# Performance work log

Hardware: AMD Instinct MI355X
Metric: run time of the kernel (lower is better)

## Reference

```python
import jax, jax.numpy as jnp
import numpy as np

B, TA, TV, D, H = 4, 1024, 1024, 512, 8
HD = D // H
SCALE = HD ** -0.5
LN_EPS = 1e-5


def setup_inputs() -> dict:
    key = jax.random.key(0)
    ks = jax.random.split(key, 16)
    init = lambda k, shape, s: (jax.random.normal(k, shape, jnp.float32) * s)
    inp = {
        'q': jax.random.normal(ks[0], (B, TA, D), jnp.float32),
        'k': jax.random.normal(ks[1], (B, TV, D), jnp.float32),
        'v': jax.random.normal(ks[2], (B, TV, D), jnp.float32),
        'guide_map': jax.random.uniform(ks[3], (B, TA, TV), jnp.float32),
        'Wq': init(ks[4], (D, D), D ** -0.5), 'bq': jnp.zeros((D,), jnp.float32),
        'Wk': init(ks[5], (D, D), D ** -0.5), 'bk': jnp.zeros((D,), jnp.float32),
        'Wv': init(ks[6], (D, D), D ** -0.5), 'bv': jnp.zeros((D,), jnp.float32),
        'Wo': init(ks[7], (D, D), D ** -0.5), 'bo': jnp.zeros((D,), jnp.float32),
        'ln_gamma': jnp.ones((D,), jnp.float32),
        'ln_beta': jnp.zeros((D,), jnp.float32),
        'gate': jnp.zeros((1,), jnp.float32),
        'bias_scale': jnp.array(10.0, jnp.float32),
    }
    return inp


def layer_norm(x, gamma, beta):
    mu = jnp.mean(x, axis=-1, keepdims=True)
    var = jnp.mean(jnp.square(x - mu), axis=-1, keepdims=True)
    return (x - mu) * jax.lax.rsqrt(var + LN_EPS) * gamma + beta


def reference(q, k, v, guide_map, Wq, bq, Wk, bk, Wv, bv, Wo, bo, ln_gamma, ln_beta, gate, bias_scale):
    # project and split heads: [B, H, T, hd]
    Q = (q @ Wq.T + bq).reshape(B, TA, H, HD).transpose(0, 2, 1, 3)
    K = (k @ Wk.T + bk).reshape(B, TV, H, HD).transpose(0, 2, 1, 3)
    V = (v @ Wv.T + bv).reshape(B, TV, H, HD).transpose(0, 2, 1, 3)
    scores = jnp.einsum('bhqd,bhkd->bhqk', Q, K) * SCALE
    # transport bias, broadcast over heads (guide_map is [B,Ta,Tv])
    transport_bias = jnp.log(guide_map + 1e-8) * jax.nn.softplus(bias_scale)
    scores = scores + transport_bias[:, None, :, :]
    attn = jax.nn.softmax(scores, axis=-1)  # dropout is identity in eval
    context = jnp.einsum('bhqk,bhkd->bhqd', attn, V)
    context = context.transpose(0, 2, 1, 3).reshape(B, TA, D)
    out = context @ Wo.T + bo
    return layer_norm(q + jax.nn.sigmoid(gate) * out, ln_gamma, ln_beta)
```

## Files before the change

kernel.cpp:

```cpp
#include <hip/hip_runtime.h>
#include <hip/hip_bf16.h>
#include <math.h>

typedef __bf16 bf16_t;
typedef _Float16 hf16_t;
typedef bf16_t bf16x8 __attribute__((ext_vector_type(8)));
typedef bf16_t bf16x4 __attribute__((ext_vector_type(4)));
typedef hf16_t hf16x8 __attribute__((ext_vector_type(8)));
typedef float f32x4 __attribute__((ext_vector_type(4)));
typedef short s16x4 __attribute__((ext_vector_type(4)));

#define B_  4
#define TA_ 1024
#define TV_ 1024
#define D_  512
#define H_  8
#define HD_ 64
#define SCALE_ 0.125f

__device__ inline void g2l16(const void* g, void* l) {
    __builtin_amdgcn_global_load_lds(
        (const __attribute__((address_space(1))) void*)g,
        (__attribute__((address_space(3))) void*)l, 16, 0, 0);
}

__device__ inline f32x4 mfma16_bf16(bf16x4 a, bf16x4 b, f32x4 c) {
    return __builtin_amdgcn_mfma_f32_16x16x16bf16_1k(
        __builtin_bit_cast(s16x4, a), __builtin_bit_cast(s16x4, b), c, 0, 0, 0);
}

__global__ __launch_bounds__(256) void prep_all(
    const float* __restrict__ G, hf16_t* __restrict__ bias_t,
    const float* __restrict__ q, const float* __restrict__ k, const float* __restrict__ v,
    const float* __restrict__ Wq, const float* __restrict__ Wk,
    const float* __restrict__ Wv, const float* __restrict__ Wo,
    bf16_t* __restrict__ qb, bf16_t* __restrict__ kb, bf16_t* __restrict__ vb,
    bf16_t* __restrict__ Wb)
{
    const int tid = threadIdx.x;
    if (blockIdx.x < 1024) {
        __shared__ float Gt[64][68];
        const int kt = blockIdx.x & 15, q64 = (blockIdx.x >> 4) & 15, b = blockIdx.x >> 8;
        const int row = tid >> 4, col4 = (tid & 15) * 4;
        #pragma unroll
        for (int it = 0; it < 4; ++it) {
            int r = it * 16 + row;
            f32x4 g = *(const f32x4*)(G + ((size_t)(b * TA_ + q64 * 64 + r)) * TV_ + kt * 64 + col4);
            *(f32x4*)&Gt[r][col4] = g;
        }
        __syncthreads();
        const int lane = tid & 63, wave = tid >> 6, quad = lane >> 4, l16 = lane & 15;
        hf16x8 lo, hi;
        #pragma unroll
        for (int ct = 0; ct < 4; ++ct) {
            #pragma unroll
            for (int r = 0; r < 4; ++r) {
                float gv = Gt[wave * 16 + l16][ct * 16 + quad * 4 + r];
                float lb = __logf(gv + 1e-8f);
                int idx = ct * 4 + r;
                if (idx < 8) lo[idx] = (hf16_t)lb; else hi[idx - 8] = (hf16_t)lb;
            }
        }
        size_t doff = ((((size_t)b * 16 + kt) * 16 + q64) * 256 + tid) * 16;
        *(hf16x8*)(bias_t + doff) = lo;
        *(hf16x8*)(bias_t + doff + 8) = hi;
    } else {
        const size_t i = ((size_t)(blockIdx.x - 1024) * 256 + tid) * 8;
        const float* src; bf16_t* dst; size_t off;
        const size_t M2 = (size_t)1 << 21;
        if (i < M2)          { src = q; dst = qb; off = i; }
        else if (i < 2 * M2) { src = k; dst = kb; off = i - M2; }
        else if (i < 3 * M2) { src = v; dst = vb; off = i - 2 * M2; }
        else {
            size_t j = i - 3 * M2;
            int wsel = (int)(j >> 18); off = j & 262143;
            src = (wsel == 0) ? Wq : (wsel == 1) ? Wk : (wsel == 2) ? Wv : Wo;
            dst = Wb + ((size_t)wsel << 18);
        }
        f32x4 a = *(const f32x4*)(src + off), c = *(const f32x4*)(src + off + 4);
        bf16x8 r;
        #pragma unroll
        for (int t = 0; t < 4; ++t) { r[t] = (bf16_t)a[t]; r[t + 4] = (bf16_t)c[t]; }
        *(bf16x8*)(dst + off) = r;
    }
}

__device__ inline void gemm128_core(
    const bf16_t* __restrict__ X, const bf16_t* __restrict__ W,
    int mbase, int nbase, bf16_t (*__restrict__ Asm)[128 * 32],
    bf16_t (*__restrict__ Bsm)[128 * 32], f32x4 acc[4][4])
{
    const int tid  = threadIdx.x;
    const int wave = tid >> 6, lane = tid & 63;
    const int quad = lane >> 4, l16 = lane & 15;
    const int wm = wave & 1, wn = wave >> 1;
    const int srow = lane >> 2;
    const int scol = (lane & 3) * 8;

    auto stage = [&](int kt, int buf) {
        const int k0 = kt * 32;
        #pragma unroll
        for (int i = 0; i < 2; ++i) {
            const int row = wave * 32 + i * 16;
            g2l16(X + (size_t)(mbase + row + srow) * D_ + k0 + scol,
                  &Asm[buf][row * 32] + (size_t)lane * 8);
            g2l16(W + (size_t)(nbase + row + srow) * D_ + k0 + scol,
                  &Bsm[buf][row * 32] + (size_t)lane * 8);
        }
    };

    stage(0, 0);
    __syncthreads();
    for (int kt = 0; kt < 16; ++kt) {
        const int buf = kt & 1;
        if (kt < 15) stage(kt + 1, buf ^ 1);
        bf16x8 af[4], bf_[4];
        #pragma unroll
        for (int t = 0; t < 4; ++t) {
            af[t]  = *(const bf16x8*)&Asm[buf][(wm * 64 + t * 16 + l16) * 32 + quad * 8];
            bf_[t] = *(const bf16x8*)&Bsm[buf][(wn * 64 + t * 16 + l16) * 32 + quad * 8];
        }
        #pragma unroll
        for (int mt = 0; mt < 4; ++mt) {
            #pragma unroll
            for (int nt = 0; nt < 4; ++nt)
                acc[mt][nt] = __builtin_amdgcn_mfma_f32_16x16x32_bf16(af[mt], bf_[nt], acc[mt][nt], 0, 0, 0);
        }
        __syncthreads();
    }
}

__global__ __launch_bounds__(256) void gemm_qkv(
    const bf16_t* __restrict__ qb, const bf16_t* __restrict__ kb, const bf16_t* __restrict__ vb,
    const bf16_t* __restrict__ Wb,
    const float* __restrict__ bq, const float* __restrict__ bk, const float* __restrict__ bv,
    bf16_t* __restrict__ Qp, bf16_t* __restrict__ Kp, bf16_t* __restrict__ Vt)
{
    __shared__ bf16_t Asm[2][128 * 32];
    __shared__ bf16_t Bsm[2][128 * 32];

    const int tid  = threadIdx.x;
    const int wave = tid >> 6, lane = tid & 63;
    const int quad = lane >> 4, l16 = lane & 15;
    const int wm = wave & 1, wn = wave >> 1;
    const int mbase = blockIdx.x * 128, nbase = blockIdx.y * 128;
    const int z = blockIdx.z;

    const bf16_t* X   = (z == 0) ? qb : (z == 1) ? kb : vb;
    const float* bias = (z == 0) ? bq : (z == 1) ? bk : bv;
    const bf16_t* W   = Wb + ((size_t)z << 18);

    f32x4 acc[4][4] = {};
    gemm128_core(X, W, mbase, nbase, Asm, Bsm, acc);

    bf16_t* out = (z == 0) ? Qp : (z == 1) ? Kp : Vt;
    #pragma unroll
    for (int mt = 0; mt < 4; ++mt) {
        #pragma unroll
        for (int nt = 0; nt < 4; ++nt) {
            #pragma unroll
            for (int r = 0; r < 4; ++r) {
                int m = mbase + wm * 64 + mt * 16 + quad * 4 + r;
                int n = nbase + wn * 64 + nt * 16 + l16;
                float val = acc[mt][nt][r] + bias[n];
                int b = m >> 10, t = m & 1023, h = n >> 6, hd = n & 63;
                if (z != 2)
                    out[(((size_t)(b * H_ + h) * TA_) + t) * HD_ + hd] = (bf16_t)val;
                else
                    out[((size_t)(b * H_ + h) * HD_ + hd) * TV_ + t] = (bf16_t)val;
            }
        }
    }
}

__global__ __launch_bounds__(512, 4) void attn_kernel(
    const bf16_t* __restrict__ Qp, const bf16_t* __restrict__ Kp,
    const bf16_t* __restrict__ Vt, const hf16_t* __restrict__ bias_t,
    const float* __restrict__ bias_scale, bf16_t* __restrict__ ctx)
{
    __shared__ bf16_t Ksm[2][2][64][72];
    __shared__ bf16_t Vsm[2][2][64][72];

    const int tid  = threadIdx.x;
    const int wave = tid >> 6, lane = tid & 63;
    const int half = wave >> 2, w4 = wave & 3;
    const int quad = lane >> 4, l16 = lane & 15;
    const int bh = blockIdx.x, b = bh >> 3, h = bh & 7;
    const int q64 = blockIdx.y;
    const int t0 = half * 8;
    const int qbase = q64 * 64 + w4 * 16;
    const int rsub = lane >> 3, csub = lane & 7;
    const int shsrc = (lane & 48) | ((lane >> 2) & 12);

    const float sp = log1pf(__expf(bias_scale[0]));

    bf16x8 aq[2];
    #pragma unroll
    for (int s = 0; s < 2; ++s)
        aq[s] = *(const bf16x8*)(Qp + ((size_t)bh * TA_ + qbase + l16) * HD_ + s * 32 + quad * 8);

    f32x4 o[4] = {};
    float m_ = -1e30f, l_ = 0.f;

    auto issue_kv = [&](int kt, bf16x8 kr[2], bf16x8 vr[2]) {
        const int kbase = kt * 64;
        #pragma unroll
        for (int i = 0; i < 2; ++i) {
            int row = w4 * 16 + i * 8 + rsub;
            kr[i] = *(const bf16x8*)(Kp + ((size_t)bh * TV_ + kbase + row) * HD_ + csub * 8);
            vr[i] = *(const bf16x8*)(Vt + ((size_t)bh * HD_ + row) * TV_ + kbase + csub * 8);
        }
    };
    auto write_kv = [&](int buf, bf16x8 kr[2], bf16x8 vr[2]) {
        #pragma unroll
        for (int i = 0; i < 2; ++i) {
            int row = w4 * 16 + i * 8 + rsub;
            *(bf16x8*)&Ksm[half][buf][row][csub * 8] = kr[i];
            *(bf16x8*)&Vsm[half][buf][row][csub * 8] = vr[i];
        }
    };

    const int tidb = (w4 << 6) | lane;
    const hf16_t* bias_base = bias_t + (((size_t)b * 16 * 16 + q64) * 256 + tidb) * 16;
    auto bias_ld = [&](int kt, hf16x8& lo, hf16x8& hi) {
        const hf16_t* bp = bias_base + (size_t)kt * 65536;
        lo = *(const hf16x8*)bp;
        hi = *(const hf16x8*)(bp + 8);
    };
    hf16x8 b0lo, b0hi, b1lo, b1hi;
    bias_ld(t0, b0lo, b0hi);
    bias_ld(t0 + 1, b1lo, b1hi);

    {
        bf16x8 kr[2], vr[2];
        issue_kv(t0, kr, vr);
        write_kv(0, kr, vr);
    }
    __syncthreads();

    auto tile_body = [&](int lk, int buf, hf16x8& slo, hf16x8& shi) {
        const int kt = t0 + lk;
        bf16x8 krn[2], vrn[2];
        if (lk < 7) issue_kv(kt + 1, krn, vrn);
        hf16x8 clo = slo, chi = shi;
        if (lk < 6) bias_ld(kt + 2, slo, shi);

        f32x4 st[4];
        #pragma unroll
        for (int ct = 0; ct < 4; ++ct) {
            f32x4 acc = {};
            #pragma unroll
            for (int s = 0; s < 2; ++s) {
                bf16x8 bk = *(const bf16x8*)&Ksm[half][buf][ct * 16 + l16][s * 32 + quad * 8];
                acc = __builtin_amdgcn_mfma_f32_16x16x32_bf16(bk, aq[s], acc, 0, 0, 0);
            }
            st[ct] = acc;
        }
        float sv[4][4], mx = -1e30f;
        #pragma unroll
        for (int ct = 0; ct < 4; ++ct) {
            #pragma unroll
            for (int r = 0; r < 4; ++r) {
                int idx = ct * 4 + r;
                float lb = (idx < 8) ? (float)clo[idx] : (float)chi[idx - 8];
                float val = fmaf(lb, sp, st[ct][r] * SCALE_);
                sv[ct][r] = val;
                mx = fmaxf(mx, val);
            }
        }
        mx = fmaxf(mx, __shfl_xor(mx, 16, 64));
        mx = fmaxf(mx, __shfl_xor(mx, 32, 64));
        float mn = fmaxf(m_, mx);
        float alpha = __expf(m_ - mn);
        m_ = mn;
        float ls = 0.f;
        #pragma unroll
        for (int ct = 0; ct < 4; ++ct) {
            #pragma unroll
            for (int r = 0; r < 4; ++r) {
                float p = __expf(sv[ct][r] - mn);
                sv[ct][r] = p;
                ls += p;
            }
        }
        ls += __shfl_xor(ls, 16, 64);
        ls += __shfl_xor(ls, 32, 64);
        l_ = l_ * alpha + ls;
        #pragma unroll
        for (int r = 0; r < 4; ++r) {
            float af = __shfl(alpha, shsrc | r, 64);
            #pragma unroll
            for (int dt = 0; dt < 4; ++dt) o[dt][r] *= af;
        }
        #pragma unroll
        for (int ct = 0; ct < 4; ++ct) {
            bf16x4 ap;
            #pragma unroll
            for (int r = 0; r < 4; ++r) ap[r] = (bf16_t)sv[ct][r];
            #pragma unroll
            for (int dt = 0; dt < 4; ++dt) {
                bf16x4 bv = *(const bf16x4*)&Vsm[half][buf][dt * 16 + l16][ct * 16 + quad * 4];
                o[dt] = mfma16_bf16(ap, bv, o[dt]);
            }
        }
        if (lk < 7) write_kv(buf ^ 1, krn, vrn);
        __syncthreads();
    };

    #pragma unroll 1
    for (int kk = 0; kk < 8; kk += 2) {
        tile_body(kk,     0, b0lo, b0hi);
        tile_body(kk + 1, 1, b1lo, b1hi);
    }

    float* cb = (float*)&Ksm[0][0][0][0];
    if (half == 1) {
        float* p = cb + (size_t)tidb * 18;
        #pragma unroll
        for (int dt = 0; dt < 4; ++dt) {
            #pragma unroll
            for (int r = 0; r < 4; ++r) p[dt * 4 + r] = o[dt][r];
        }
        p[16] = m_; p[17] = l_;
    }
    __syncthreads();
    if (half == 0) {
        const float* p = cb + (size_t)tidb * 18;
        float s0[4], s1[4];
        #pragma unroll
        for (int r = 0; r < 4; ++r) {
            float m0 = __shfl(m_, shsrc | r, 64);
            float l0 = __shfl(l_, shsrc | r, 64);
            const float* pr = cb + (size_t)((w4 << 6) | (shsrc | r)) * 18;
            float m1 = pr[16], l1 = pr[17];
            float mm = fmaxf(m0, m1);
            float e0 = __expf(m0 - mm), e1 = __expf(m1 - mm);
            float L = l0 * e0 + l1 * e1;
            s0[r] = e0 / L; s1[r] = e1 / L;
        }
        #pragma unroll
        for (int dt = 0; dt < 4; ++dt) {
            #pragma unroll
            for (int r = 0; r < 4; ++r) {
                float v = o[dt][r] * s0[r] + p[dt * 4 + r] * s1[r];
                int qrow = q64 * 64 + w4 * 16 + quad * 4 + r;
                ctx[((size_t)b * TA_ + qrow) * D_ + h * HD_ + dt * 16 + l16] = (bf16_t)v;
            }
        }
    }
}

__global__ __launch_bounds__(512) void gemm_out_ln(
    const bf16_t* __restrict__ ctx, const bf16_t* __restrict__ Wob,
    const float* __restrict__ bo, const float* __restrict__ q,
    const float* __restrict__ gamma, const float* __restrict__ beta,
    const float* __restrict__ gate, float* __restrict__ y)
{
    __shared__ bf16_t Asm[2][32 * 32];
    __shared__ bf16_t Bsm[2][512 * 32];
    __shared__ float ps[32][4], psq[32][4];

    const int tid  = threadIdx.x;
    const int wave = tid >> 6, lane = tid & 63;
    const int quad = lane >> 4, l16 = lane & 15;
    const int tg = wave & 1, nh = wave >> 1;
    const int mbase = blockIdx.x * 32;

    auto stage = [&](int kt, int buf) {
        const int k0 = kt * 32;
        #pragma unroll
        for (int j = 0; j < 4; ++j) {
            int row0 = wave * 64 + j * 16;
            g2l16(Wob + (size_t)(row0 + (lane >> 2)) * D_ + k0 + (lane & 3) * 8,
                  &Bsm[buf][row0 * 32] + (size_t)lane * 8);
        }
        if (wave < 2) {
            int row0 = wave * 16;
            g2l16(ctx + (size_t)(mbase + row0 + (lane >> 2)) * D_ + k0 + (lane & 3) * 8,
                  &Asm[buf][row0 * 32] + (size_t)lane * 8);
        }
    };

    f32x4 acc[8] = {};
    stage(0, 0);
    __syncthreads();
    for (int kt = 0; kt < 16; ++kt) {
        const int buf = kt & 1;
        if (kt < 15) stage(kt + 1, buf ^ 1);
        bf16x8 af = *(const bf16x8*)&Asm[buf][(tg * 16 + l16) * 32 + quad * 8];
        #pragma unroll
        for (int nt = 0; nt < 8; ++nt) {
            bf16x8 bf_ = *(const bf16x8*)&Bsm[buf][(nh * 128 + nt * 16 + l16) * 32 + quad * 8];
            acc[nt] = __builtin_amdgcn_mfma_f32_16x16x32_bf16(af, bf_, acc[nt], 0, 0, 0);
        }
        __syncthreads();
    }

    const float sg = 1.f / (1.f + __expf(-gate[0]));
    float s[4] = {0.f, 0.f, 0.f, 0.f}, sq[4] = {0.f, 0.f, 0.f, 0.f};
    #pragma unroll
    for (int nt = 0; nt < 8; ++nt) {
        int n = nh * 128 + nt * 16 + l16;
        float bon = bo[n];
        #pragma unroll
        for (int r = 0; r < 4; ++r) {
            int m = mbase + tg * 16 + quad * 4 + r;
            float x = q[(size_t)m * D_ + n] + sg * (acc[nt][r] + bon);
            acc[nt][r] = x;
            s[r] += x; sq[r] += x * x;
        }
    }
    #pragma unroll
    for (int off = 1; off < 16; off <<= 1) {
        #pragma unroll
        for (int r = 0; r < 4; ++r) {
            s[r]  += __shfl_xor(s[r],  off, 64);
            sq[r] += __shfl_xor(sq[r], off, 64);
        }
    }
    if (l16 == 0) {
        #pragma unroll
        for (int r = 0; r < 4; ++r) {
            ps[tg * 16 + quad * 4 + r][nh]  = s[r];
            psq[tg * 16 + quad * 4 + r][nh] = sq[r];
        }
    }
    __syncthreads();
    float mu[4], rstd[4];
    #pragma unroll
    for (int r = 0; r < 4; ++r) {
        int row = tg * 16 + quad * 4 + r;
        float S  = ps[row][0] + ps[row][1] + ps[row][2] + ps[row][3];
        float SQ = psq[row][0] + psq[row][1] + psq[row][2] + psq[row][3];
        mu[r] = S * (1.f / D_);
        float var = SQ * (1.f / D_) - mu[r] * mu[r];
        rstd[r] = rsqrtf(var + 1e-5f);
    }
    #pragma unroll
    for (int nt = 0; nt < 8; ++nt) {
        int n = nh * 128 + nt * 16 + l16;
        float gn = gamma[n], bn = beta[n];
        #pragma unroll
        for (int r = 0; r < 4; ++r) {
            int m = mbase + tg * 16 + quad * 4 + r;
            y[(size_t)m * D_ + n] = (acc[nt][r] - mu[r]) * rstd[r] * gn + bn;
        }
    }
}

extern "C" void kernel_launch(void* const* d_in, const int* in_sizes, int n_in,
                              void* d_out, int out_size, void* d_ws, size_t ws_size,
                              hipStream_t stream) {
    const float* q       = (const float*)d_in[0];
    const float* k       = (const float*)d_in[1];
    const float* v       = (const float*)d_in[2];
    const float* guide   = (const float*)d_in[3];
    const float* Wq      = (const float*)d_in[4];
    const float* bq      = (const float*)d_in[5];
    const float* Wk      = (const float*)d_in[6];
    const float* bk      = (const float*)d_in[7];
    const float* Wv      = (const float*)d_in[8];
    const float* bv      = (const float*)d_in[9];
    const float* Wo      = (const float*)d_in[10];
    const float* bo      = (const float*)d_in[11];
    const float* gamma   = (const float*)d_in[12];
    const float* beta    = (const float*)d_in[13];
    const float* gate    = (const float*)d_in[14];
    const float* bscale  = (const float*)d_in[15];

    char* w = (char*)d_ws;
    bf16_t* qb     = (bf16_t*)(w);
    bf16_t* kb     = (bf16_t*)(w + (4u  << 20));
    bf16_t* vb     = (bf16_t*)(w + (8u  << 20));
    bf16_t* Wb     = (bf16_t*)(w + (12u << 20));
    bf16_t* Qp     = (bf16_t*)(w + (14u << 20));
    bf16_t* Kp     = (bf16_t*)(w + (18u << 20));
    bf16_t* Vt     = (bf16_t*)(w + (22u << 20));
    bf16_t* ctx    = (bf16_t*)(w + (26u << 20));
    hf16_t* bias_t = (hf16_t*)(w + (30u << 20));

    prep_all<<<4608, 256, 0, stream>>>(guide, bias_t, q, k, v, Wq, Wk, Wv, Wo, qb, kb, vb, Wb);
    gemm_qkv<<<dim3(32, 4, 3), 256, 0, stream>>>(qb, kb, vb, Wb, bq, bk, bv, Qp, Kp, Vt);
    attn_kernel<<<dim3(32, 16), 512, 0, stream>>>(Qp, Kp, Vt, bias_t, bscale, ctx);
    gemm_out_ln<<<128, 512, 0, stream>>>(ctx, Wb + ((size_t)3 << 18), bo, q,
                                         gamma, beta, gate, (float*)d_out);
}
```

Baseline: 176.0 us.

## Fold softmax scale into Q, use exp2, defer rescaling, prioritize MFMA waves

Q projection output is pre-multiplied by scale*log2e, and the bias multiplier also absorbs log2e, so the softmax can use a raw exp2 instruction without a per-element scale. Online-softmax rescaling of the accumulator is skipped unless the running max grows past a threshold in some lane of the wave. MFMA sections get raised wave priority, and the V-transposed store in the projection epilogue is vectorized to bf16x4. Deferring the max update risks bf16 overflow or precision loss if scores exceed the threshold range, and storing Q pre-scaled changes its bf16 rounding.

```diff
diff --git a/kernel.cpp b/kernel.cpp
--- a/kernel.cpp
+++ b/kernel.cpp
@@ -17,6 +17,11 @@
 #define H_  8
 #define HD_ 64
 #define SCALE_ 0.125f
+#define LOG2E_ 1.442695041f
+#define QSCALE_ 0.1803368801f
+#define DEFER_THR_ 11.5416f
+
+__device__ inline float fast_exp2(float x) { return __builtin_amdgcn_exp2f(x); }
 
 __device__ inline void g2l16(const void* g, void* l) {
     __builtin_amdgcn_global_load_lds(
@@ -158,16 +163,24 @@
     for (int mt = 0; mt < 4; ++mt) {
         #pragma unroll
         for (int nt = 0; nt < 4; ++nt) {
-            #pragma unroll
-            for (int r = 0; r < 4; ++r) {
-                int m = mbase + wm * 64 + mt * 16 + quad * 4 + r;
-                int n = nbase + wn * 64 + nt * 16 + l16;
-                float val = acc[mt][nt][r] + bias[n];
-                int b = m >> 10, t = m & 1023, h = n >> 6, hd = n & 63;
-                if (z != 2)
+            const int n = nbase + wn * 64 + nt * 16 + l16;
+            const float bn = bias[n];
+            if (z == 2) {
+                int m0 = mbase + wm * 64 + mt * 16 + quad * 4;
+                int b = m0 >> 10, t = m0 & 1023, h = n >> 6, hd = n & 63;
+                bf16x4 pk;
+                #pragma unroll
+                for (int r = 0; r < 4; ++r) pk[r] = (bf16_t)(acc[mt][nt][r] + bn);
+                *(bf16x4*)(out + ((size_t)(b * H_ + h) * HD_ + hd) * TV_ + t) = pk;
+            } else {
+                #pragma unroll
+                for (int r = 0; r < 4; ++r) {
+                    int m = mbase + wm * 64 + mt * 16 + quad * 4 + r;
+                    float val = acc[mt][nt][r] + bn;
+                    if (z == 0) val *= QSCALE_;
+                    int b = m >> 10, t = m & 1023, h = n >> 6, hd = n & 63;
                     out[(((size_t)(b * H_ + h) * TA_) + t) * HD_ + hd] = (bf16_t)val;
-                else
-                    out[((size_t)(b * H_ + h) * HD_ + hd) * TV_ + t] = (bf16_t)val;
+                }
             }
         }
     }
@@ -192,7 +205,7 @@
     const int rsub = lane >> 3, csub = lane & 7;
     const int shsrc = (lane & 48) | ((lane >> 2) & 12);
 
-    const float sp = log1pf(__expf(bias_scale[0]));
+    const float sp = log1pf(__expf(bias_scale[0])) * LOG2E_;
 
     bf16x8 aq[2];
     #pragma unroll
@@ -246,6 +259,7 @@
         if (lk < 6) bias_ld(kt + 2, slo, shi);
 
         f32x4 st[4];
+        __builtin_amdgcn_s_setprio(1);
         #pragma unroll
         for (int ct = 0; ct < 4; ++ct) {
             f32x4 acc = {};
@@ -256,6 +270,7 @@
             }
             st[ct] = acc;
         }
+        __builtin_amdgcn_s_setprio(0);
         float sv[4][4], mx = -1e30f;
         #pragma unroll
         for (int ct = 0; ct < 4; ++ct) {
@@ -263,35 +278,42 @@
             for (int r = 0; r < 4; ++r) {
                 int idx = ct * 4 + r;
                 float lb = (idx < 8) ? (float)clo[idx] : (float)chi[idx - 8];
-                float val = fmaf(lb, sp, st[ct][r] * SCALE_);
+                float val = fmaf(lb, sp, st[ct][r]);
                 sv[ct][r] = val;
                 mx = fmaxf(mx, val);
             }
         }
         mx = fmaxf(mx, __shfl_xor(mx, 16, 64));
         mx = fmaxf(mx, __shfl_xor(mx, 32, 64));
-        float mn = fmaxf(m_, mx);
-        float alpha = __expf(m_ - mn);
-        m_ = mn;
+        float mn;
+        if (__all(mx - m_ <= DEFER_THR_)) {
+            mn = m_;
+        } else {
+            mn = fmaxf(m_, mx);
+            float alpha = fast_exp2(m_ - mn);
+            m_ = mn;
+            l_ *= alpha;
+            #pragma unroll
+            for (int r = 0; r < 4; ++r) {
+                float af = __shfl(alpha, shsrc | r, 64);
+                #pragma unroll
+                for (int dt = 0; dt < 4; ++dt) o[dt][r] *= af;
+            }
+        }
         float ls = 0.f;
         #pragma unroll
         for (int ct = 0; ct < 4; ++ct) {
             #pragma unroll
             for (int r = 0; r < 4; ++r) {
-                float p = __expf(sv[ct][r] - mn);
+                float p = fast_exp2(sv[ct][r] - mn);
                 sv[ct][r] = p;
                 ls += p;
             }
         }
         ls += __shfl_xor(ls, 16, 64);
         ls += __shfl_xor(ls, 32, 64);
-        l_ = l_ * alpha + ls;
-        #pragma unroll
-        for (int r = 0; r < 4; ++r) {
-            float af = __shfl(alpha, shsrc | r, 64);
-            #pragma unroll
-            for (int dt = 0; dt < 4; ++dt) o[dt][r] *= af;
-        }
+        l_ += ls;
+        __builtin_amdgcn_s_setprio(1);
         #pragma unroll
         for (int ct = 0; ct < 4; ++ct) {
             bf16x4 ap;
@@ -303,6 +325,7 @@
                 o[dt] = mfma16_bf16(ap, bv, o[dt]);
             }
         }
+        __builtin_amdgcn_s_setprio(0);
         if (lk < 7) write_kv(buf ^ 1, krn, vrn);
         __syncthreads();
     };
@@ -334,7 +357,7 @@
             const float* pr = cb + (size_t)((w4 << 6) | (shsrc | r)) * 18;
             float m1 = pr[16], l1 = pr[17];
             float mm = fmaxf(m0, m1);
-            float e0 = __expf(m0 - mm), e1 = __expf(m1 - mm);
+            float e0 = fast_exp2(m0 - mm), e1 = fast_exp2(m1 - mm);
             float L = l0 * e0 + l1 * e1;
             s0[r] = e0 / L; s1[r] = e1 / L;
         }
```

Measured after the change: 174.3 us. No clear change (-1.0%).
